# Kernel optimization log

Hardware: AMD Instinct MI355X
Metric: run time of the kernel (lower is better)

Reference implementation:

```python
import jax, jax.numpy as jnp
import numpy as np

B, T, DKQ, DV, EKQ, EV, H, OUT = 8, 2048, 64, 64, 128, 128, 4, 32
FF = 4 * EV
NEG = -1e30  # additive mask value (safe stand-in for -inf)


def _ln(x, g, b, eps=1e-5):
    m = x.mean(-1, keepdims=True)
    var = ((x - m) ** 2).mean(-1, keepdims=True)
    return (x - m) * jax.lax.rsqrt(var + eps) * g + b


def _attn(q, k, v, mask):
    # q,k,v: [n, T, E] -> heads [n, H, T, dh]; NOTE: no 1/sqrt(d) scaling (faithful to source)
    n, t, _ = q.shape
    q = q.reshape(n, t, H, -1).transpose(0, 2, 1, 3)
    k = k.reshape(n, t, H, -1).transpose(0, 2, 1, 3)
    v = v.reshape(n, t, H, -1).transpose(0, 2, 1, 3)
    w = jnp.einsum('bhqd,bhkd->bhqk', q, k) + mask  # [n,H,T,T]
    a = jax.nn.softmax(w, axis=-1)
    o = jnp.einsum('bhqk,bhkd->bhqd', a, v)
    return o.transpose(0, 2, 1, 3).reshape(n, t, -1)


def setup_inputs() -> dict:
    key = jax.random.key(0)
    ks = jax.random.split(key, 32)
    w = lambda k, s: jax.random.normal(k, s, jnp.float32) * 0.02
    DIN_A = DKQ + DV
    return {
        'kq': jax.random.normal(ks[0], (B, T, DKQ), jnp.float32),
        'v': jax.random.normal(ks[1], (B, T, DV), jnp.float32),
        # Layer A (input_dim = DKQ+DV, embed = EV)
        'A_Wk': w(ks[2], (DIN_A, EV)), 'A_bk': jnp.zeros((EV,), jnp.float32),
        'A_Wq': w(ks[3], (DIN_A, EV)), 'A_bq': jnp.zeros((EV,), jnp.float32),
        'A_Wv': w(ks[4], (DIN_A, EV)), 'A_bv': jnp.zeros((EV,), jnp.float32),
        'A_f1W': w(ks[5], (EV, FF)), 'A_f1b': jnp.zeros((FF,), jnp.float32),
        'A_f2W': w(ks[6], (FF, EV)), 'A_f2b': jnp.zeros((EV,), jnp.float32),
        'A_n1g': jnp.ones((EV,), jnp.float32), 'A_n1b': jnp.zeros((EV,), jnp.float32),
        'A_n2g': jnp.ones((EV,), jnp.float32), 'A_n2b': jnp.zeros((EV,), jnp.float32),
        # Layer B (kq -> EKQ, vA -> EV)
        'B_Wk': w(ks[7], (DKQ, EKQ)), 'B_bk': jnp.zeros((EKQ,), jnp.float32),
        'B_Wq': w(ks[8], (DKQ, EKQ)), 'B_bq': jnp.zeros((EKQ,), jnp.float32),
        'B_Wv': w(ks[9], (EV, EV)), 'B_bv': jnp.zeros((EV,), jnp.float32),
        'B_f1W': w(ks[10], (EV, FF)), 'B_f1b': jnp.zeros((FF,), jnp.float32),
        'B_f2W': w(ks[11], (FF, EV)), 'B_f2b': jnp.zeros((EV,), jnp.float32),
        # Output head
        'out_W': w(ks[12], (EV, OUT)), 'out_b': jnp.zeros((OUT,), jnp.float32),
    }


def reference(kq, v, A_Wk, A_bk, A_Wq, A_bq, A_Wv, A_bv, A_f1W, A_f1b, A_f2W, A_f2b,
              A_n1g, A_n1b, A_n2g, A_n2b, B_Wk, B_bk, B_Wq, B_bq, B_Wv, B_bv,
              B_f1W, B_f1b, B_f2W, B_f2b, out_W, out_b):
    n, t, _ = kq.shape
    i = jnp.arange(t)[:, None]
    j = jnp.arange(t)[None, :]
    mask_a = jnp.where(j <= i, 0.0, NEG).astype(jnp.float32)               # causal (diag=1)
    mask_b = jnp.where((j < i) | ((i == 0) & (j == 0)), 0.0, NEG).astype(jnp.float32)  # strict causal + (0,0) exception

    # ---- Layer A ----
    X = jnp.concatenate([kq, v], axis=-1)
    K = X @ A_Wk + A_bk
    Q = X @ A_Wq + A_bq
    V = X @ A_Wv + A_bv
    attn_out = _attn(Q, K, V, mask_a)
    h1 = _ln(V + attn_out, A_n1g, A_n1b)
    ff = jax.nn.gelu(h1 @ A_f1W + A_f1b, approximate=False) @ A_f2W + A_f2b
    vA = _ln(h1 + ff, A_n2g, A_n2b)

    # ---- Layer B (no residuals / norms: values is overwritten in source) ----
    K2 = kq @ B_Wk + B_bk
    Q2 = kq @ B_Wq + B_bq
    V2 = vA @ B_Wv + B_bv
    attn_out2 = _attn(Q2, K2, V2, mask_b)
    ff2 = jax.nn.gelu(attn_out2 @ B_f1W + B_f1b, approximate=False) @ B_f2W + B_f2b

    return ff2 @ out_W + out_b
```

## Files before the change

kernel.cpp:

```cpp
#include <hip/hip_runtime.h>
#include <hip/hip_bf16.h>

#define TSEQ 2048
#define NBATCH 8
#define NROWS (NBATCH*TSEQ)
#define EMB 128
#define NH 4
#define DH 32
#define OUTD 32
#define APLANE (NROWS*EMB)
#define LOG2E 1.4426950408889634f

typedef short s8v __attribute__((ext_vector_type(8)));
typedef short s4v __attribute__((ext_vector_type(4)));
typedef float f4v __attribute__((ext_vector_type(4)));

__device__ __forceinline__ unsigned short f2bf(float f){
  unsigned int u = __float_as_uint(f);
  unsigned int r = u + 0x7fffu + ((u >> 16) & 1u);
  return (unsigned short)(r >> 16);
}
__device__ __forceinline__ float bf2f(unsigned short u){
  return __uint_as_float(((unsigned int)u) << 16);
}

struct WPack {
  const float* src[10];
  int off[10];
  int ntk[10];
  int rowoff[10];
  int nsh[10];
  int kn[10];
};
__global__ __launch_bounds__(256) void prep_w(WPack p, short* __restrict__ warena){
  int blk = blockIdx.x, m = 0;
  #pragma unroll
  for (int i=0;i<10;i++){
    int nb = p.kn[i] >> 8;
    if (blk < nb){ m = i; break; }
    blk -= nb;
  }
  int idx = blk*256 + threadIdx.x;
  float x = p.src[m][idx];
  int nsh = p.nsh[m];
  int n = idx & ((1<<nsh)-1);
  int k = idx >> nsh;
  int K = p.kn[m] >> nsh;
  unsigned short hi = f2bf(x);
  unsigned short lo = f2bf(x - bf2f(hi));
  short* dh = warena + p.off[m] + (size_t)(p.rowoff[m] + n)*K + k;
  dh[0]        = (short)hi;
  dh[p.ntk[m]] = (short)lo;
}

__global__ __launch_bounds__(256) void prep_wc(const float* __restrict__ f2W, const float* __restrict__ f2b,
                                               const float* __restrict__ oW, const float* __restrict__ ob,
                                               float* __restrict__ Wc, float* __restrict__ bc){
  int idx = blockIdx.x*256 + threadIdx.x;
  if (idx < 512*32){
    int k = idx >> 5, n = idx & 31;
    float s = 0.f;
    #pragma unroll 4
    for (int j=0;j<128;j++) s = fmaf(f2W[k*128+j], oW[j*32+n], s);
    Wc[idx] = s;
  } else if (idx < 512*32 + 32){
    int n = idx - 512*32;
    float s = ob[n];
    for (int j=0;j<128;j++) s = fmaf(f2b[j], oW[j*32+n], s);
    bc[n] = s;
  }
}

__global__ __launch_bounds__(256) void xsplit(const float* __restrict__ kq, const float* __restrict__ v,
                                              unsigned short* __restrict__ X){
  int idx = blockIdx.x*256 + threadIdx.x;
  int row = idx >> 7, c = idx & 127;
  float val = (c < 64) ? kq[row*64 + c] : v[row*64 + (c-64)];
  unsigned short hi = f2bf(val);
  X[idx]          = hi;
  X[idx + APLANE] = f2bf(val - bf2f(hi));
}

struct GOuts {
  const float* bias[3];
  float* of[3];
  unsigned short* ob[3];
  unsigned short* vt[3];
  float scale[3];
};
__global__ __launch_bounds__(256) void gemm2(
    const unsigned short* __restrict__ A, int aplane, int lda, int K, int niter,
    const short* __restrict__ wt, int NTK,
    GOuts og, int NT, int nseg, int act){
  __shared__ short As[2][2][64*40];
  const int tid  = threadIdx.x;
  const int w    = tid >> 6;
  const int lane = tid & 63;
  const int col  = lane & 15;
  const int quad = lane >> 4;
  const int row0 = blockIdx.x * 64;
  const int colg = blockIdx.y*64 + w*16 + col;
  const bool two = (aplane != 0);

  f4v acc[4];
  #pragma unroll
  for (int i=0;i<4;i++) acc[i] = (f4v){0.f,0.f,0.f,0.f};

  const int ar = tid >> 2, ac = (tid & 3)*8;
  const unsigned short* abase = A + (size_t)(row0 + ar)*lda;
  const short* wbase = wt + (size_t)colg*K + quad*8;

  s8v pah, pal, pbh, pbl;
  pah = *(const s8v*)(abase + ac);
  if (two) pal = *(const s8v*)(abase + aplane + ac);
  pbh = *(const s8v*)(wbase);
  pbl = *(const s8v*)(wbase + NTK);

  for (int i=0;i<niter;i++){
    const int buf = i & 1;
    *(s8v*)&As[buf][0][ar*40 + ac] = pah;
    if (two) *(s8v*)&As[buf][1][ar*40 + ac] = pal;
    __syncthreads();
    s8v bh = pbh, bl = pbl;
    if (i+1 < niter){
      const int kcol = (i+1)*32;
      pah = *(const s8v*)(abase + kcol + ac);
      if (two) pal = *(const s8v*)(abase + aplane + kcol + ac);
      pbh = *(const s8v*)(wbase + kcol);
      pbl = *(const s8v*)(wbase + NTK + kcol);
    }
    #pragma unroll
    for (int rt=0;rt<4;rt++){
      s8v ah = *(const s8v*)&As[buf][0][(rt*16 + col)*40 + quad*8];
      acc[rt] = __builtin_amdgcn_mfma_f32_16x16x32_bf16(ah, bh, acc[rt], 0, 0, 0);
      if (two){
        s8v al = *(const s8v*)&As[buf][1][(rt*16 + col)*40 + quad*8];
        acc[rt] = __builtin_amdgcn_mfma_f32_16x16x32_bf16(al, bh, acc[rt], 0, 0, 0);
      }
      acc[rt] = __builtin_amdgcn_mfma_f32_16x16x32_bf16(ah, bl, acc[rt], 0, 0, 0);
    }
  }

  int seg, lcol, ldc;
  if (nseg > 1){ seg = colg >> 7; lcol = colg & 127; ldc = 128; }
  else         { seg = 0; lcol = colg; ldc = NT; }
  const float bv = og.bias[seg][lcol];
  const float sc = og.scale[seg];
  float* of = og.of[seg];
  unsigned short* ob = og.ob[seg];
  unsigned short* vtp = og.vt[seg];
  float vals[4][4];
  #pragma unroll
  for (int rt=0;rt<4;rt++){
    #pragma unroll
    for (int r=0;r<4;r++){
      float val = acc[rt][r] + bv;
      if (act == 1) val = 0.5f*val*(1.f + erff(val*0.70710678118654752440f));
      vals[rt][r] = val * sc;
    }
  }
  #pragma unroll
  for (int rt=0;rt<4;rt++){
    const int row = row0 + rt*16 + quad*4;
    #pragma unroll
    for (int r=0;r<4;r++){
      if (ob)      ob[(size_t)(row+r)*ldc + lcol] = f2bf(vals[rt][r]);
      else if (of) of[(size_t)(row+r)*ldc + lcol] = vals[rt][r];
    }
  }
  if (vtp){
    const int hh = lcol >> 5, dd = lcol & 31;
    const int bb = row0 >> 11;
    unsigned short* vbase = vtp + ((size_t)(bb*NH + hh)*32 + dd)*TSEQ + (row0 & (TSEQ-1)) + quad*4;
    #pragma unroll
    for (int rt=0;rt<4;rt++){
      s4v pk;
      #pragma unroll
      for (int r=0;r<4;r++) pk[r] = (short)f2bf(vals[rt][r]);
      *(s4v*)(vbase + rt*16) = pk;
    }
  }
}

#define KT_STRIDE 40
#define VT_STRIDE 72
#define PW_STRIDE 72
__global__ __launch_bounds__(128) void flash3(const unsigned short* __restrict__ Qb,
                                              const unsigned short* __restrict__ Kb,
                                              const unsigned short* __restrict__ Vtb,
                                              float* __restrict__ O0, float* __restrict__ O1,
                                              float* __restrict__ L0, float* __restrict__ L1,
                                              int mode){
  __shared__ short Kt[64*KT_STRIDE];
  __shared__ short Vt[32*VT_STRIDE];
  __shared__ short Pw[2][16*PW_STRIDE];
  const int tid  = threadIdx.x;
  const int w    = tid >> 6;
  const int lane = tid & 63;
  const int col  = lane & 15;
  const int quad = lane >> 4;
  const int bh = blockIdx.y;
  const int b = bh >> 2, h = bh & 3;
  const int par = blockIdx.z;
  float* Op = par ? O1 : O0;
  float* Lp = par ? L1 : L0;
  const int kr = tid >> 1, kc16 = (tid & 1)*16;
  const int vd = tid >> 2, vk16 = (tid & 3)*16;

  for (int pass = 0; pass < 2; pass++){
    const int t = pass ? blockIdx.x : (63 - blockIdx.x);
    const int qbase = t*32 + w*16;
    const int jtmax = t >> 1;
    const int qg = qbase + col;

    s8v qf = *(const s8v*)(Qb + (size_t)(b*TSEQ + qg)*EMB + h*DH + quad*8);
    f4v o0 = {0.f,0.f,0.f,0.f}, o1 = {0.f,0.f,0.f,0.f};
    float lsum = 0.f;

    if (par <= jtmax){
      s8v ka, kb2, va, vb;
      {
        const unsigned short* kp = Kb + (size_t)(b*TSEQ + par*64 + kr)*EMB + h*DH + kc16;
        ka = *(const s8v*)kp; kb2 = *(const s8v*)(kp + 8);
        const unsigned short* vp = Vtb + ((size_t)bh*32 + vd)*TSEQ + par*64 + vk16;
        va = *(const s8v*)vp; vb = *(const s8v*)(vp + 8);
      }
      for (int jt = par; jt <= jtmax; jt += 2){
        __syncthreads();
        *(s8v*)&Kt[kr*KT_STRIDE + kc16]     = ka;
        *(s8v*)&Kt[kr*KT_STRIDE + kc16 + 8] = kb2;
        *(s8v*)&Vt[vd*VT_STRIDE + vk16]     = va;
        *(s8v*)&Vt[vd*VT_STRIDE + vk16 + 8] = vb;
        __syncthreads();
        if (jt + 2 <= jtmax){
          const unsigned short* kp = Kb + (size_t)(b*TSEQ + (jt+2)*64 + kr)*EMB + h*DH + kc16;
          ka = *(const s8v*)kp; kb2 = *(const s8v*)(kp + 8);
          const unsigned short* vp = Vtb + ((size_t)bh*32 + vd)*TSEQ + (jt+2)*64 + vk16;
          va = *(const s8v*)vp; vb = *(const s8v*)(vp + 8);
        }
        f4v s[4];
        #pragma unroll
        for (int t4=0;t4<4;t4++){
          s8v kf = *(const s8v*)&Kt[(t4*16 + col)*KT_STRIDE + quad*8];
          f4v z = {0.f,0.f,0.f,0.f};
          s[t4] = __builtin_amdgcn_mfma_f32_16x16x32_bf16(kf, qf, z, 0, 0, 0);
        }
        if (jt == jtmax){
          const int j0 = jt*64;
          #pragma unroll
          for (int t4=0;t4<4;t4++){
            #pragma unroll
            for (int r=0;r<4;r++){
              const int jg = j0 + t4*16 + quad*4 + r;
              const bool ok = (mode==0) ? (jg <= qg) : ((jg < qg) || (qg==0 && jg==0));
              s[t4][r] = ok ? s[t4][r] : -1e30f;
            }
          }
        }
        #pragma unroll
        for (int t4=0;t4<4;t4++){
          s4v pk;
          #pragma unroll
          for (int r=0;r<4;r++){
            float pv = exp2f(s[t4][r]);
            lsum += pv;
            pk[r] = (short)f2bf(pv);
          }
          *(s4v*)&Pw[w][col*PW_STRIDE + t4*16 + quad*4] = pk;
        }
        #pragma unroll
        for (int kk=0;kk<2;kk++){
          s8v pf  = *(const s8v*)&Pw[w][col*PW_STRIDE + kk*32 + quad*8];
          s8v vf0 = *(const s8v*)&Vt[(col)*VT_STRIDE    + kk*32 + quad*8];
          s8v vf1 = *(const s8v*)&Vt[(16+col)*VT_STRIDE + kk*32 + quad*8];
          o0 = __builtin_amdgcn_mfma_f32_16x16x32_bf16(vf0, pf, o0, 0, 0, 0);
          o1 = __builtin_amdgcn_mfma_f32_16x16x32_bf16(vf1, pf, o1, 0, 0, 0);
        }
      }
    }
    lsum += __shfl_xor(lsum, 16);
    lsum += __shfl_xor(lsum, 32);
    float* obase = Op + (size_t)(b*TSEQ + qg)*EMB + h*DH + quad*4;
    *(float4*)(obase)      = make_float4(o0[0],o0[1],o0[2],o0[3]);
    *(float4*)(obase + 16) = make_float4(o1[0],o1[1],o1[2],o1[3]);
    if (quad == 0) Lp[(size_t)(b*TSEQ + qg)*NH + h] = lsum;
  }
}

__global__ __launch_bounds__(64) void combine_ln(const float* __restrict__ O0, const float* __restrict__ O1,
                                                 const float* __restrict__ L0, const float* __restrict__ L1,
                                                 const float* __restrict__ Vf,
                                                 const float* __restrict__ g, const float* __restrict__ bt,
                                                 unsigned short* __restrict__ outp){
  const int row = blockIdx.x;
  const int tid = threadIdx.x;
  const size_t base = (size_t)row*EMB;
  const int h0 = tid >> 5, h1i = 2 + (tid >> 5);
  const float la = L0[(size_t)row*NH + h0] + L1[(size_t)row*NH + h0];
  const float lb = L0[(size_t)row*NH + h1i] + L1[(size_t)row*NH + h1i];
  float x0 = Vf[base+tid]    + (O0[base+tid]    + O1[base+tid])    / la;
  float x1 = Vf[base+tid+64] + (O0[base+tid+64] + O1[base+tid+64]) / lb;
  float s  = x0 + x1;
  float s2 = x0*x0 + x1*x1;
  #pragma unroll
  for (int off=1; off<64; off<<=1){
    s  += __shfl_xor(s,  off);
    s2 += __shfl_xor(s2, off);
  }
  float mean = s * (1.f/128.f);
  float var  = s2 * (1.f/128.f) - mean*mean;
  float rstd = rsqrtf(var + 1e-5f);
  float y0 = (x0-mean)*rstd*g[tid]    + bt[tid];
  float y1 = (x1-mean)*rstd*g[tid+64] + bt[tid+64];
  unsigned short h0b = f2bf(y0), h1b = f2bf(y1);
  outp[base+tid]             = h0b;
  outp[base+tid+64]          = h1b;
  outp[base+tid+APLANE]      = f2bf(y0 - bf2f(h0b));
  outp[base+tid+64+APLANE]   = f2bf(y1 - bf2f(h1b));
}

__global__ __launch_bounds__(64) void ln2(const unsigned short* __restrict__ Xp, const float* __restrict__ R,
                                          const float* __restrict__ g, const float* __restrict__ bt,
                                          unsigned short* __restrict__ outp){
  const int row = blockIdx.x;
  const int tid = threadIdx.x;
  const size_t base = (size_t)row*EMB;
  float x0 = bf2f(Xp[base+tid])    + bf2f(Xp[base+tid+APLANE])    + R[base+tid];
  float x1 = bf2f(Xp[base+tid+64]) + bf2f(Xp[base+tid+64+APLANE]) + R[base+tid+64];
  float s  = x0 + x1;
  float s2 = x0*x0 + x1*x1;
  #pragma unroll
  for (int off=1; off<64; off<<=1){
    s  += __shfl_xor(s,  off);
    s2 += __shfl_xor(s2, off);
  }
  float mean = s * (1.f/128.f);
  float var  = s2 * (1.f/128.f) - mean*mean;
  float rstd = rsqrtf(var + 1e-5f);
  float y0 = (x0-mean)*rstd*g[tid]    + bt[tid];
  float y1 = (x1-mean)*rstd*g[tid+64] + bt[tid+64];
  unsigned short h0b = f2bf(y0), h1b = f2bf(y1);
  outp[base+tid]             = h0b;
  outp[base+tid+64]          = h1b;
  outp[base+tid+APLANE]      = f2bf(y0 - bf2f(h0b));
  outp[base+tid+64+APLANE]   = f2bf(y1 - bf2f(h1b));
}

__global__ __launch_bounds__(256) void combine_b(const float* __restrict__ O0, const float* __restrict__ O1,
                                                 const float* __restrict__ L0, const float* __restrict__ L1,
                                                 unsigned short* __restrict__ outp){
  const int idx = blockIdx.x*256 + threadIdx.x;
  const int row = idx >> 7, c = idx & 127, h = c >> 5;
  const float l = L0[(size_t)row*NH + h] + L1[(size_t)row*NH + h];
  const float v = (O0[idx] + O1[idx]) / l;
  unsigned short hb = f2bf(v);
  outp[idx]          = hb;
  outp[idx + APLANE] = f2bf(v - bf2f(hb));
}

__global__ __launch_bounds__(256) void out2(const unsigned short* __restrict__ mid,
                                            const float* __restrict__ Wc, const float* __restrict__ bc,
                                            float* __restrict__ out){
  __shared__ float As[8*512];
  const int tid = threadIdx.x;
  const int row0 = blockIdx.x*8;
  for (int idx = tid; idx < 8*512; idx += 256)
    As[idx] = bf2f(mid[(size_t)row0*512 + idx]);
  __syncthreads();
  const int r = tid >> 5, c = tid & 31;
  float acc = bc[c];
  const float* as = &As[r*512];
  #pragma unroll 8
  for (int k=0;k<512;k++) acc = fmaf(as[k], Wc[k*32+c], acc);
  out[(size_t)(row0+r)*OUTD + c] = acc;
}

extern "C" void kernel_launch(void* const* d_in, const int* in_sizes, int n_in,
                              void* d_out, int out_size, void* d_ws, size_t ws_size,
                              hipStream_t stream) {
  const float* kq    = (const float*)d_in[0];
  const float* v     = (const float*)d_in[1];
  const float* A_Wk  = (const float*)d_in[2];  const float* A_bk  = (const float*)d_in[3];
  const float* A_Wq  = (const float*)d_in[4];  const float* A_bq  = (const float*)d_in[5];
  const float* A_Wv  = (const float*)d_in[6];  const float* A_bv  = (const float*)d_in[7];
  const float* A_f1W = (const float*)d_in[8];  const float* A_f1b = (const float*)d_in[9];
  const float* A_f2W = (const float*)d_in[10]; const float* A_f2b = (const float*)d_in[11];
  const float* A_n1g = (const float*)d_in[12]; const float* A_n1b = (const float*)d_in[13];
  const float* A_n2g = (const float*)d_in[14]; const float* A_n2b = (const float*)d_in[15];
  const float* B_Wk  = (const float*)d_in[16]; const float* B_bk  = (const float*)d_in[17];
  const float* B_Wq  = (const float*)d_in[18]; const float* B_bq  = (const float*)d_in[19];
  const float* B_Wv  = (const float*)d_in[20]; const float* B_bv  = (const float*)d_in[21];
  const float* B_f1W = (const float*)d_in[22]; const float* B_f1b = (const float*)d_in[23];
  const float* B_f2W = (const float*)d_in[24]; const float* B_f2b = (const float*)d_in[25];
  const float* out_W = (const float*)d_in[26]; const float* out_b = (const float*)d_in[27];
  float* out = (float*)d_out;
  (void)in_sizes; (void)n_in; (void)out_size; (void)ws_size;

  char* ws = (char*)d_ws;
  const size_t MB = 1024*1024;
  short* warena = (short*)ws;
  float* Wc  = (float*)(ws + 1536*1024);
  float* bc  = (float*)(ws + 1536*1024 + 65536);
  unsigned short* Xs  = (unsigned short*)(ws + 2*MB);
  unsigned short* Qbf = (unsigned short*)(ws + 10*MB);
  unsigned short* Kbf = (unsigned short*)(ws + 14*MB);
  unsigned short* Vtb = (unsigned short*)(ws + 18*MB);
  float* Vf  = (float*)(ws + 22*MB);
  float* O0  = (float*)(ws + 30*MB);
  float* O1  = (float*)(ws + 38*MB);
  float* L0  = (float*)(ws + 46*MB);
  float* L1  = (float*)(ws + 47*MB);
  unsigned short* h1p = (unsigned short*)(ws + 48*MB);
  unsigned short* mid = (unsigned short*)(ws + 56*MB);
  float* ffo = (float*)(ws + 72*MB);
  unsigned short* vAp = (unsigned short*)(ws + 80*MB);

  WPack p;
  const float* srcs[10] = {A_Wq,A_Wk,A_Wv,A_f1W,A_f2W,B_Wq,B_Wk,B_Wv,B_f1W,B_f2W};
  int kn[10]     = {16384,16384,16384,65536,65536,8192,8192,16384,65536,65536};
  int nsh[10]    = {7,7,7,9,7,7,7,7,9,7};
  int off[10]    = {0,0,0,98304,229376,360448,360448,393216,425984,557056};
  int ntk[10]    = {49152,49152,49152,65536,65536,16384,16384,16384,65536,65536};
  int rowoff[10] = {0,128,256,0,0,0,128,0,0,0};
  int nblk = 0;
  for (int i=0;i<10;i++){
    p.src[i]=srcs[i]; p.kn[i]=kn[i]; p.nsh[i]=nsh[i];
    p.off[i]=off[i]; p.ntk[i]=ntk[i]; p.rowoff[i]=rowoff[i];
    nblk += kn[i] >> 8;
  }
  prep_w<<<nblk, 256, 0, stream>>>(p, warena);
  prep_wc<<<65, 256, 0, stream>>>(B_f2W, B_f2b, out_W, out_b, Wc, bc);
  xsplit<<<NROWS*128/256, 256, 0, stream>>>(kq, v, Xs);

  GOuts oQKVA = {{A_bq,A_bk,A_bv},{nullptr,nullptr,Vf},{Qbf,Kbf,nullptr},{nullptr,nullptr,Vtb},{LOG2E,1.f,1.f}};
  GOuts oF1A  = {{A_f1b,nullptr,nullptr},{nullptr,nullptr,nullptr},{mid,nullptr,nullptr},{nullptr,nullptr,nullptr},{1.f,1.f,1.f}};
  GOuts oF2A  = {{A_f2b,nullptr,nullptr},{ffo,nullptr,nullptr},{nullptr,nullptr,nullptr},{nullptr,nullptr,nullptr},{1.f,1.f,1.f}};
  GOuts oQKB  = {{B_bq,B_bk,nullptr},{nullptr,nullptr,nullptr},{Qbf,Kbf,nullptr},{nullptr,nullptr,nullptr},{LOG2E,1.f,1.f}};
  GOuts oVB   = {{B_bv,nullptr,nullptr},{nullptr,nullptr,nullptr},{nullptr,nullptr,nullptr},{Vtb,nullptr,nullptr},{1.f,1.f,1.f}};
  GOuts oF1B  = {{B_f1b,nullptr,nullptr},{nullptr,nullptr,nullptr},{mid,nullptr,nullptr},{nullptr,nullptr,nullptr},{1.f,1.f,1.f}};

  gemm2<<<dim3(256,6), 256, 0, stream>>>(Xs, APLANE, 128, 128, 4, warena + 0,      49152, oQKVA, 384, 3, 0);
  flash3<<<dim3(32,32,2), 128, 0, stream>>>(Qbf, Kbf, Vtb, O0, O1, L0, L1, 0);
  combine_ln<<<NROWS, 64, 0, stream>>>(O0, O1, L0, L1, Vf, A_n1g, A_n1b, h1p);
  gemm2<<<dim3(256,8), 256, 0, stream>>>(h1p, APLANE, 128, 128, 4, warena + 98304, 65536, oF1A, 512, 1, 1);
  gemm2<<<dim3(256,2), 256, 0, stream>>>(mid, 0,      512, 512, 16, warena + 229376, 65536, oF2A, 128, 1, 0);
  ln2<<<NROWS, 64, 0, stream>>>(h1p, ffo, A_n2g, A_n2b, vAp);

  gemm2<<<dim3(256,4), 256, 0, stream>>>(Xs, APLANE, 128, 64, 2,  warena + 360448, 16384, oQKB, 256, 2, 0);
  gemm2<<<dim3(256,2), 256, 0, stream>>>(vAp, APLANE, 128, 128, 4, warena + 393216, 16384, oVB, 128, 1, 0);
  flash3<<<dim3(32,32,2), 128, 0, stream>>>(Qbf, Kbf, Vtb, O0, O1, L0, L1, 1);
  combine_b<<<NROWS*128/256, 256, 0, stream>>>(O0, O1, L0, L1, h1p);
  gemm2<<<dim3(256,8), 256, 0, stream>>>(h1p, APLANE, 128, 128, 4, warena + 425984, 65536, oF1B, 512, 1, 1);
  out2<<<NROWS/8, 256, 0, stream>>>(mid, Wc, bc, out);
}
```

Baseline: 333.1 us.

## Split attention KV into four partitions, share K/V tiles across paired query tiles

```diff
diff --git a/kernel.cpp b/kernel.cpp
--- a/kernel.cpp
+++ b/kernel.cpp
@@ -85,7 +85,6 @@
   const float* bias[3];
   float* of[3];
   unsigned short* ob[3];
-  unsigned short* vt[3];
   float scale[3];
 };
 __global__ __launch_bounds__(256) void gemm2(
@@ -148,48 +147,49 @@
   const float sc = og.scale[seg];
   float* of = og.of[seg];
   unsigned short* ob = og.ob[seg];
-  unsigned short* vtp = og.vt[seg];
-  float vals[4][4];
   #pragma unroll
   for (int rt=0;rt<4;rt++){
     #pragma unroll
     for (int r=0;r<4;r++){
+      const int row = row0 + rt*16 + quad*4 + r;
       float val = acc[rt][r] + bv;
       if (act == 1) val = 0.5f*val*(1.f + erff(val*0.70710678118654752440f));
-      vals[rt][r] = val * sc;
+      val *= sc;
+      if (ob) ob[(size_t)row*ldc + lcol] = f2bf(val);
+      if (of) of[(size_t)row*ldc + lcol] = val;
     }
   }
+}
+
+__global__ __launch_bounds__(256) void vtrans2(const unsigned short* __restrict__ Vbf,
+                                               unsigned short* __restrict__ Vtb){
+  __shared__ short Lt[64*40];
+  const int tid = threadIdx.x;
+  const int t0 = blockIdx.x * 64;
+  const int bh = blockIdx.y;
+  const int b = bh >> 2, h = bh & 3;
+  {
+    const int r = tid >> 2, c = (tid & 3)*8;
+    *(s8v*)&Lt[r*40 + c] = *(const s8v*)(Vbf + (size_t)(b*TSEQ + t0 + r)*EMB + h*DH + c);
+  }
+  __syncthreads();
+  const int d = tid >> 3, kc = (tid & 7)*8;
+  s8v o;
   #pragma unroll
-  for (int rt=0;rt<4;rt++){
-    const int row = row0 + rt*16 + quad*4;
-    #pragma unroll
-    for (int r=0;r<4;r++){
-      if (ob)      ob[(size_t)(row+r)*ldc + lcol] = f2bf(vals[rt][r]);
-      else if (of) of[(size_t)(row+r)*ldc + lcol] = vals[rt][r];
-    }
-  }
-  if (vtp){
-    const int hh = lcol >> 5, dd = lcol & 31;
-    const int bb = row0 >> 11;
-    unsigned short* vbase = vtp + ((size_t)(bb*NH + hh)*32 + dd)*TSEQ + (row0 & (TSEQ-1)) + quad*4;
-    #pragma unroll
-    for (int rt=0;rt<4;rt++){
-      s4v pk;
-      #pragma unroll
-      for (int r=0;r<4;r++) pk[r] = (short)f2bf(vals[rt][r]);
-      *(s4v*)(vbase + rt*16) = pk;
-    }
-  }
+  for (int j=0;j<8;j++) o[j] = Lt[(kc + j)*40 + d];
+  *(s8v*)(Vtb + ((size_t)bh*32 + d)*TSEQ + t0 + kc) = o;
 }
 
 #define KT_STRIDE 40
 #define VT_STRIDE 72
 #define PW_STRIDE 72
-__global__ __launch_bounds__(128) void flash3(const unsigned short* __restrict__ Qb,
+__global__ __launch_bounds__(128) void flash4(const unsigned short* __restrict__ Qb,
                                               const unsigned short* __restrict__ Kb,
                                               const unsigned short* __restrict__ Vtb,
                                               float* __restrict__ O0, float* __restrict__ O1,
+                                              float* __restrict__ O2, float* __restrict__ O3,
                                               float* __restrict__ L0, float* __restrict__ L1,
+                                              float* __restrict__ L2, float* __restrict__ L3,
                                               int mode){
   __shared__ short Kt[64*KT_STRIDE];
   __shared__ short Vt[32*VT_STRIDE];
@@ -202,93 +202,144 @@
   const int bh = blockIdx.y;
   const int b = bh >> 2, h = bh & 3;
   const int par = blockIdx.z;
-  float* Op = par ? O1 : O0;
-  float* Lp = par ? L1 : L0;
+  float* Op = (par==0) ? O0 : (par==1) ? O1 : (par==2) ? O2 : O3;
+  float* Lp = (par==0) ? L0 : (par==1) ? L1 : (par==2) ? L2 : L3;
   const int kr = tid >> 1, kc16 = (tid & 1)*16;
   const int vd = tid >> 2, vk16 = (tid & 3)*16;
 
-  for (int pass = 0; pass < 2; pass++){
-    const int t = pass ? blockIdx.x : (63 - blockIdx.x);
-    const int qbase = t*32 + w*16;
-    const int jtmax = t >> 1;
-    const int qg = qbase + col;
-
-    s8v qf = *(const s8v*)(Qb + (size_t)(b*TSEQ + qg)*EMB + h*DH + quad*8);
-    f4v o0 = {0.f,0.f,0.f,0.f}, o1 = {0.f,0.f,0.f,0.f};
-    float lsum = 0.f;
-
-    if (par <= jtmax){
-      s8v ka, kb2, va, vb;
-      {
-        const unsigned short* kp = Kb + (size_t)(b*TSEQ + par*64 + kr)*EMB + h*DH + kc16;
-        ka = *(const s8v*)kp; kb2 = *(const s8v*)(kp + 8);
-        const unsigned short* vp = Vtb + ((size_t)bh*32 + vd)*TSEQ + par*64 + vk16;
-        va = *(const s8v*)vp; vb = *(const s8v*)(vp + 8);
-      }
-      for (int jt = par; jt <= jtmax; jt += 2){
-        __syncthreads();
-        *(s8v*)&Kt[kr*KT_STRIDE + kc16]     = ka;
-        *(s8v*)&Kt[kr*KT_STRIDE + kc16 + 8] = kb2;
-        *(s8v*)&Vt[vd*VT_STRIDE + vk16]     = va;
-        *(s8v*)&Vt[vd*VT_STRIDE + vk16 + 8] = vb;
-        __syncthreads();
-        if (jt + 2 <= jtmax){
-          const unsigned short* kp = Kb + (size_t)(b*TSEQ + (jt+2)*64 + kr)*EMB + h*DH + kc16;
-          ka = *(const s8v*)kp; kb2 = *(const s8v*)(kp + 8);
-          const unsigned short* vp = Vtb + ((size_t)bh*32 + vd)*TSEQ + (jt+2)*64 + vk16;
-          va = *(const s8v*)vp; vb = *(const s8v*)(vp + 8);
-        }
-        f4v s[4];
+  const int tA = 63 - blockIdx.x, tB = blockIdx.x;
+  const int jtA = tA >> 1, jtB = tB >> 1;
+  const int qA = tA*32 + w*16 + col;
+  const int qB = tB*32 + w*16 + col;
+
+  s8v qfA = *(const s8v*)(Qb + (size_t)(b*TSEQ + qA)*EMB + h*DH + quad*8);
+  s8v qfB = *(const s8v*)(Qb + (size_t)(b*TSEQ + qB)*EMB + h*DH + quad*8);
+  f4v oA0 = {0,0,0,0}, oA1 = {0,0,0,0}, oB0 = {0,0,0,0}, oB1 = {0,0,0,0};
+  float lsA = 0.f, lsB = 0.f;
+
+  s8v ka, kb2, va, vb;
+  {
+    const unsigned short* kp = Kb + (size_t)(b*TSEQ + par*64 + kr)*EMB + h*DH + kc16;
+    ka = *(const s8v*)kp; kb2 = *(const s8v*)(kp + 8);
+    const unsigned short* vp = Vtb + ((size_t)bh*32 + vd)*TSEQ + par*64 + vk16;
+    va = *(const s8v*)vp; vb = *(const s8v*)(vp + 8);
+  }
+
+  for (int jt = par; jt <= jtA; jt += 4){
+    __syncthreads();
+    *(s8v*)&Kt[kr*KT_STRIDE + kc16]     = ka;
+    *(s8v*)&Kt[kr*KT_STRIDE + kc16 + 8] = kb2;
+    *(s8v*)&Vt[vd*VT_STRIDE + vk16]     = va;
+    *(s8v*)&Vt[vd*VT_STRIDE + vk16 + 8] = vb;
+    __syncthreads();
+    if (jt + 4 <= jtA){
+      const unsigned short* kp = Kb + (size_t)(b*TSEQ + (jt+4)*64 + kr)*EMB + h*DH + kc16;
+      ka = *(const s8v*)kp; kb2 = *(const s8v*)(kp + 8);
+      const unsigned short* vp = Vtb + ((size_t)bh*32 + vd)*TSEQ + (jt+4)*64 + vk16;
+      va = *(const s8v*)vp; vb = *(const s8v*)(vp + 8);
+    }
+    s8v vr00 = *(const s8v*)&Vt[(col)*VT_STRIDE + quad*8];
+    s8v vr01 = *(const s8v*)&Vt[(16+col)*VT_STRIDE + quad*8];
+    s8v vr10 = *(const s8v*)&Vt[(col)*VT_STRIDE + 32 + quad*8];
+    s8v vr11 = *(const s8v*)&Vt[(16+col)*VT_STRIDE + 32 + quad*8];
+    s8v kf0 = *(const s8v*)&Kt[(col)*KT_STRIDE + quad*8];
+    s8v kf1 = *(const s8v*)&Kt[(16+col)*KT_STRIDE + quad*8];
+    s8v kf2 = *(const s8v*)&Kt[(32+col)*KT_STRIDE + quad*8];
+    s8v kf3 = *(const s8v*)&Kt[(48+col)*KT_STRIDE + quad*8];
+
+    {
+      f4v s[4];
+      f4v z = {0,0,0,0};
+      s[0] = __builtin_amdgcn_mfma_f32_16x16x32_bf16(kf0, qfA, z, 0, 0, 0);
+      s[1] = __builtin_amdgcn_mfma_f32_16x16x32_bf16(kf1, qfA, z, 0, 0, 0);
+      s[2] = __builtin_amdgcn_mfma_f32_16x16x32_bf16(kf2, qfA, z, 0, 0, 0);
+      s[3] = __builtin_amdgcn_mfma_f32_16x16x32_bf16(kf3, qfA, z, 0, 0, 0);
+      if (jt == jtA){
+        const int j0 = jt*64;
         #pragma unroll
         for (int t4=0;t4<4;t4++){
-          s8v kf = *(const s8v*)&Kt[(t4*16 + col)*KT_STRIDE + quad*8];
-          f4v z = {0.f,0.f,0.f,0.f};
-          s[t4] = __builtin_amdgcn_mfma_f32_16x16x32_bf16(kf, qf, z, 0, 0, 0);
-        }
-        if (jt == jtmax){
-          const int j0 = jt*64;
           #pragma unroll
-          for (int t4=0;t4<4;t4++){
-            #pragma unroll
-            for (int r=0;r<4;r++){
-              const int jg = j0 + t4*16 + quad*4 + r;
-              const bool ok = (mode==0) ? (jg <= qg) : ((jg < qg) || (qg==0 && jg==0));
-              s[t4][r] = ok ? s[t4][r] : -1e30f;
-            }
+          for (int r=0;r<4;r++){
+            const int jg = j0 + t4*16 + quad*4 + r;
+            const bool ok = (mode==0) ? (jg <= qA) : ((jg < qA) || (qA==0 && jg==0));
+            s[t4][r] = ok ? s[t4][r] : -1e30f;
           }
         }
+      }
+      #pragma unroll
+      for (int t4=0;t4<4;t4++){
+        s4v pk;
+        #pragma unroll
+        for (int r=0;r<4;r++){
+          float pv = exp2f(s[t4][r]);
+          lsA += pv;
+          pk[r] = (short)f2bf(pv);
+        }
+        *(s4v*)&Pw[w][col*PW_STRIDE + t4*16 + quad*4] = pk;
+      }
+      s8v pf0 = *(const s8v*)&Pw[w][col*PW_STRIDE + quad*8];
+      s8v pf1 = *(const s8v*)&Pw[w][col*PW_STRIDE + 32 + quad*8];
+      oA0 = __builtin_amdgcn_mfma_f32_16x16x32_bf16(vr00, pf0, oA0, 0, 0, 0);
+      oA1 = __builtin_amdgcn_mfma_f32_16x16x32_bf16(vr01, pf0, oA1, 0, 0, 0);
+      oA0 = __builtin_amdgcn_mfma_f32_16x16x32_bf16(vr10, pf1, oA0, 0, 0, 0);
+      oA1 = __builtin_amdgcn_mfma_f32_16x16x32_bf16(vr11, pf1, oA1, 0, 0, 0);
+    }
+    if (jt <= jtB){
+      f4v s[4];
+      f4v z = {0,0,0,0};
+      s[0] = __builtin_amdgcn_mfma_f32_16x16x32_bf16(kf0, qfB, z, 0, 0, 0);
+      s[1] = __builtin_amdgcn_mfma_f32_16x16x32_bf16(kf1, qfB, z, 0, 0, 0);
+      s[2] = __builtin_amdgcn_mfma_f32_16x16x32_bf16(kf2, qfB, z, 0, 0, 0);
+      s[3] = __builtin_amdgcn_mfma_f32_16x16x32_bf16(kf3, qfB, z, 0, 0, 0);
+      if (jt == jtB){
+        const int j0 = jt*64;
         #pragma unroll
         for (int t4=0;t4<4;t4++){
-          s4v pk;
           #pragma unroll
           for (int r=0;r<4;r++){
-            float pv = exp2f(s[t4][r]);
-            lsum += pv;
-            pk[r] = (short)f2bf(pv);
+            const int jg = j0 + t4*16 + quad*4 + r;
+            const bool ok = (mode==0) ? (jg <= qB) : ((jg < qB) || (qB==0 && jg==0));
+            s[t4][r] = ok ? s[t4][r] : -1e30f;
           }
-          *(s4v*)&Pw[w][col*PW_STRIDE + t4*16 + quad*4] = pk;
-        }
-        #pragma unroll
-        for (int kk=0;kk<2;kk++){
-          s8v pf  = *(const s8v*)&Pw[w][col*PW_STRIDE + kk*32 + quad*8];
-          s8v vf0 = *(const s8v*)&Vt[(col)*VT_STRIDE    + kk*32 + quad*8];
-          s8v vf1 = *(const s8v*)&Vt[(16+col)*VT_STRIDE + kk*32 + quad*8];
-          o0 = __builtin_amdgcn_mfma_f32_16x16x32_bf16(vf0, pf, o0, 0, 0, 0);
-          o1 = __builtin_amdgcn_mfma_f32_16x16x32_bf16(vf1, pf, o1, 0, 0, 0);
         }
       }
+      #pragma unroll
+      for (int t4=0;t4<4;t4++){
+        s4v pk;
+        #pragma unroll
+        for (int r=0;r<4;r++){
+          float pv = exp2f(s[t4][r]);
+          lsB += pv;
+          pk[r] = (short)f2bf(pv);
+        }
+        *(s4v*)&Pw[w][col*PW_STRIDE + t4*16 + quad*4] = pk;
+      }
+      s8v pf0 = *(const s8v*)&Pw[w][col*PW_STRIDE + quad*8];
+      s8v pf1 = *(const s8v*)&Pw[w][col*PW_STRIDE + 32 + quad*8];
+      oB0 = __builtin_amdgcn_mfma_f32_16x16x32_bf16(vr00, pf0, oB0, 0, 0, 0);
+      oB1 = __builtin_amdgcn_mfma_f32_16x16x32_bf16(vr01, pf0, oB1, 0, 0, 0);
+      oB0 = __builtin_amdgcn_mfma_f32_16x16x32_bf16(vr10, pf1, oB0, 0, 0, 0);
+      oB1 = __builtin_amdgcn_mfma_f32_16x16x32_bf16(vr11, pf1, oB1, 0, 0, 0);
     }
-    lsum += __shfl_xor(lsum, 16);
-    lsum += __shfl_xor(lsum, 32);
-    float* obase = Op + (size_t)(b*TSEQ + qg)*EMB + h*DH + quad*4;
-    *(float4*)(obase)      = make_float4(o0[0],o0[1],o0[2],o0[3]);
-    *(float4*)(obase + 16) = make_float4(o1[0],o1[1],o1[2],o1[3]);
-    if (quad == 0) Lp[(size_t)(b*TSEQ + qg)*NH + h] = lsum;
+  }
+  lsA += __shfl_xor(lsA, 16); lsA += __shfl_xor(lsA, 32);
+  lsB += __shfl_xor(lsB, 16); lsB += __shfl_xor(lsB, 32);
+  float* oa = Op + (size_t)(b*TSEQ + qA)*EMB + h*DH + quad*4;
+  *(float4*)(oa)      = make_float4(oA0[0],oA0[1],oA0[2],oA0[3]);
+  *(float4*)(oa + 16) = make_float4(oA1[0],oA1[1],oA1[2],oA1[3]);
+  float* obp = Op + (size_t)(b*TSEQ + qB)*EMB + h*DH + quad*4;
+  *(float4*)(obp)      = make_float4(oB0[0],oB0[1],oB0[2],oB0[3]);
+  *(float4*)(obp + 16) = make_float4(oB1[0],oB1[1],oB1[2],oB1[3]);
+  if (quad == 0){
+    Lp[(size_t)(b*TSEQ + qA)*NH + h] = lsA;
+    Lp[(size_t)(b*TSEQ + qB)*NH + h] = lsB;
   }
 }
 
 __global__ __launch_bounds__(64) void combine_ln(const float* __restrict__ O0, const float* __restrict__ O1,
+                                                 const float* __restrict__ O2, const float* __restrict__ O3,
                                                  const float* __restrict__ L0, const float* __restrict__ L1,
+                                                 const float* __restrict__ L2, const float* __restrict__ L3,
                                                  const float* __restrict__ Vf,
                                                  const float* __restrict__ g, const float* __restrict__ bt,
                                                  unsigned short* __restrict__ outp){
@@ -296,10 +347,11 @@
   const int tid = threadIdx.x;
   const size_t base = (size_t)row*EMB;
   const int h0 = tid >> 5, h1i = 2 + (tid >> 5);
-  const float la = L0[(size_t)row*NH + h0] + L1[(size_t)row*NH + h0];
-  const float lb = L0[(size_t)row*NH + h1i] + L1[(size_t)row*NH + h1i];
-  float x0 = Vf[base+tid]    + (O0[base+tid]    + O1[base+tid])    / la;
-  float x1 = Vf[base+tid+64] + (O0[base+tid+64] + O1[base+tid+64]) / lb;
+  const size_t lb0 = (size_t)row*NH;
+  const float la = L0[lb0+h0] + L1[lb0+h0] + L2[lb0+h0] + L3[lb0+h0];
+  const float lb = L0[lb0+h1i] + L1[lb0+h1i] + L2[lb0+h1i] + L3[lb0+h1i];
+  float x0 = Vf[base+tid]    + (O0[base+tid]    + O1[base+tid]    + O2[base+tid]    + O3[base+tid])    / la;
+  float x1 = Vf[base+tid+64] + (O0[base+tid+64] + O1[base+tid+64] + O2[base+tid+64] + O3[base+tid+64]) / lb;
   float s  = x0 + x1;
   float s2 = x0*x0 + x1*x1;
   #pragma unroll
@@ -347,12 +399,15 @@
 }
 
 __global__ __launch_bounds__(256) void combine_b(const float* __restrict__ O0, const float* __restrict__ O1,
+                                                 const float* __restrict__ O2, const float* __restrict__ O3,
                                                  const float* __restrict__ L0, const float* __restrict__ L1,
+                                                 const float* __restrict__ L2, const float* __restrict__ L3,
                                                  unsigned short* __restrict__ outp){
   const int idx = blockIdx.x*256 + threadIdx.x;
   const int row = idx >> 7, c = idx & 127, h = c >> 5;
-  const float l = L0[(size_t)row*NH + h] + L1[(size_t)row*NH + h];
-  const float v = (O0[idx] + O1[idx]) / l;
+  const size_t lb = (size_t)row*NH + h;
+  const float l = L0[lb] + L1[lb] + L2[lb] + L3[lb];
+  const float v = (O0[idx] + O1[idx] + O2[idx] + O3[idx]) / l;
   unsigned short hb = f2bf(v);
   outp[idx]          = hb;
   outp[idx + APLANE] = f2bf(v - bf2f(hb));
@@ -405,15 +460,20 @@
   unsigned short* Qbf = (unsigned short*)(ws + 10*MB);
   unsigned short* Kbf = (unsigned short*)(ws + 14*MB);
   unsigned short* Vtb = (unsigned short*)(ws + 18*MB);
-  float* Vf  = (float*)(ws + 22*MB);
-  float* O0  = (float*)(ws + 30*MB);
-  float* O1  = (float*)(ws + 38*MB);
-  float* L0  = (float*)(ws + 46*MB);
-  float* L1  = (float*)(ws + 47*MB);
-  unsigned short* h1p = (unsigned short*)(ws + 48*MB);
-  unsigned short* mid = (unsigned short*)(ws + 56*MB);
-  float* ffo = (float*)(ws + 72*MB);
-  unsigned short* vAp = (unsigned short*)(ws + 80*MB);
+  unsigned short* Vbf = (unsigned short*)(ws + 22*MB);
+  float* Vf  = (float*)(ws + 26*MB);
+  float* O0  = (float*)(ws + 34*MB);
+  float* O1  = (float*)(ws + 42*MB);
+  float* O2  = (float*)(ws + 50*MB);
+  float* O3  = (float*)(ws + 58*MB);
+  float* L0  = (float*)(ws + 66*MB);
+  float* L1  = (float*)(ws + 66*MB + 262144);
+  float* L2  = (float*)(ws + 66*MB + 524288);
+  float* L3  = (float*)(ws + 66*MB + 786432);
+  unsigned short* h1p = (unsigned short*)(ws + 67*MB);
+  float* ffo = (float*)(ws + 34*MB);
+  unsigned short* vAp = (unsigned short*)(ws + 42*MB);
+  unsigned short* mid = (unsigned short*)(ws + 50*MB);
 
   WPack p;
   const float* srcs[10] = {A_Wq,A_Wk,A_Wv,A_f1W,A_f2W,B_Wq,B_Wk,B_Wv,B_f1W,B_f2W};
@@ -432,24 +492,26 @@
   prep_wc<<<65, 256, 0, stream>>>(B_f2W, B_f2b, out_W, out_b, Wc, bc);
   xsplit<<<NROWS*128/256, 256, 0, stream>>>(kq, v, Xs);
 
-  GOuts oQKVA = {{A_bq,A_bk,A_bv},{nullptr,nullptr,Vf},{Qbf,Kbf,nullptr},{nullptr,nullptr,Vtb},{LOG2E,1.f,1.f}};
-  GOuts oF1A  = {{A_f1b,nullptr,nullptr},{nullptr,nullptr,nullptr},{mid,nullptr,nullptr},{nullptr,nullptr,nullptr},{1.f,1.f,1.f}};
-  GOuts oF2A  = {{A_f2b,nullptr,nullptr},{ffo,nullptr,nullptr},{nullptr,nullptr,nullptr},{nullptr,nullptr,nullptr},{1.f,1.f,1.f}};
-  GOuts oQKB  = {{B_bq,B_bk,nullptr},{nullptr,nullptr,nullptr},{Qbf,Kbf,nullptr},{nullptr,nullptr,nullptr},{LOG2E,1.f,1.f}};
-  GOuts oVB   = {{B_bv,nullptr,nullptr},{nullptr,nullptr,nullptr},{nullptr,nullptr,nullptr},{Vtb,nullptr,nullptr},{1.f,1.f,1.f}};
-  GOuts oF1B  = {{B_f1b,nullptr,nullptr},{nullptr,nullptr,nullptr},{mid,nullptr,nullptr},{nullptr,nullptr,nullptr},{1.f,1.f,1.f}};
+  GOuts oQKVA = {{A_bq,A_bk,A_bv},{nullptr,nullptr,Vf},{Qbf,Kbf,Vbf},{LOG2E,1.f,1.f}};
+  GOuts oF1A  = {{A_f1b,nullptr,nullptr},{nullptr,nullptr,nullptr},{mid,nullptr,nullptr},{1.f,1.f,1.f}};
+  GOuts oF2A  = {{A_f2b,nullptr,nullptr},{ffo,nullptr,nullptr},{nullptr,nullptr,nullptr},{1.f,1.f,1.f}};
+  GOuts oQKB  = {{B_bq,B_bk,nullptr},{nullptr,nullptr,nullptr},{Qbf,Kbf,nullptr},{LOG2E,1.f,1.f}};
+  GOuts oVB   = {{B_bv,nullptr,nullptr},{nullptr,nullptr,nullptr},{Vbf,nullptr,nullptr},{1.f,1.f,1.f}};
+  GOuts oF1B  = {{B_f1b,nullptr,nullptr},{nullptr,nullptr,nullptr},{mid,nullptr,nullptr},{1.f,1.f,1.f}};
 
   gemm2<<<dim3(256,6), 256, 0, stream>>>(Xs, APLANE, 128, 128, 4, warena + 0,      49152, oQKVA, 384, 3, 0);
-  flash3<<<dim3(32,32,2), 128, 0, stream>>>(Qbf, Kbf, Vtb, O0, O1, L0, L1, 0);
-  combine_ln<<<NROWS, 64, 0, stream>>>(O0, O1, L0, L1, Vf, A_n1g, A_n1b, h1p);
+  vtrans2<<<dim3(32,32), 256, 0, stream>>>(Vbf, Vtb);
+  flash4<<<dim3(32,32,4), 128, 0, stream>>>(Qbf, Kbf, Vtb, O0,O1,O2,O3, L0,L1,L2,L3, 0);
+  combine_ln<<<NROWS, 64, 0, stream>>>(O0,O1,O2,O3, L0,L1,L2,L3, Vf, A_n1g, A_n1b, h1p);
   gemm2<<<dim3(256,8), 256, 0, stream>>>(h1p, APLANE, 128, 128, 4, warena + 98304, 65536, oF1A, 512, 1, 1);
   gemm2<<<dim3(256,2), 256, 0, stream>>>(mid, 0,      512, 512, 16, warena + 229376, 65536, oF2A, 128, 1, 0);
   ln2<<<NROWS, 64, 0, stream>>>(h1p, ffo, A_n2g, A_n2b, vAp);
 
   gemm2<<<dim3(256,4), 256, 0, stream>>>(Xs, APLANE, 128, 64, 2,  warena + 360448, 16384, oQKB, 256, 2, 0);
   gemm2<<<dim3(256,2), 256, 0, stream>>>(vAp, APLANE, 128, 128, 4, warena + 393216, 16384, oVB, 128, 1, 0);
-  flash3<<<dim3(32,32,2), 128, 0, stream>>>(Qbf, Kbf, Vtb, O0, O1, L0, L1, 1);
-  combine_b<<<NROWS*128/256, 256, 0, stream>>>(O0, O1, L0, L1, h1p);
+  vtrans2<<<dim3(32,32), 256, 0, stream>>>(Vbf, Vtb);
+  flash4<<<dim3(32,32,4), 128, 0, stream>>>(Qbf, Kbf, Vtb, O0,O1,O2,O3, L0,L1,L2,L3, 1);
+  combine_b<<<NROWS*128/256, 256, 0, stream>>>(O0,O1,O2,O3, L0,L1,L2,L3, h1p);
   gemm2<<<dim3(256,8), 256, 0, stream>>>(h1p, APLANE, 128, 128, 4, warena + 425984, 65536, oF1B, 512, 1, 1);
   out2<<<NROWS/8, 256, 0, stream>>>(mid, Wc, bc, out);
 }
```

After: 348.3 us. +4.6%, slower.
